# Performance work log

Measured on AMD Instinct MI355X. Metric: run time of the kernel, lower is better.

The kernel has to match this reference:

```python
import jax, jax.numpy as jnp
import numpy as np

B, N, E, Q = 4, 10000, 160000, 256
D, M, U, H, P = 128, 64, 126, 128, 7  # node_dim, msg_sz, update_sz, mlp hidden, pose dim
MSG_STEPS = 3
NUM_COPIES = 1


def setup_inputs() -> dict:
    key = jax.random.key(0)
    ks = jax.random.split(key, 12)
    return {
        "nodes_states": jax.random.normal(ks[0], (B, N, D), jnp.float32),
        "query_poses": jax.random.normal(ks[1], (B, Q, P), jnp.float32),
        "attn": jax.random.uniform(ks[2], (B, Q, N), jnp.float32) / N,
        "edge_sources": jax.random.randint(ks[3], (E,), 0, N),
        "edge_sinks": jax.random.randint(ks[4], (E,), 0, N),
        "w1e": jax.random.normal(ks[5], (2 * D, H), jnp.float32) * 0.05,
        "b1e": jnp.zeros((H,), jnp.float32),
        "w2e": jax.random.normal(ks[6], (H, M), jnp.float32) * 0.05,
        "b2e": jnp.zeros((M,), jnp.float32),
        "w1n": jax.random.normal(ks[7], (D + M, H), jnp.float32) * 0.05,
        "b1n": jnp.zeros((H,), jnp.float32),
        "w2n": jax.random.normal(ks[8], (H, U), jnp.float32) * 0.05,
        "b2n": jnp.zeros((U,), jnp.float32),
    }


def reference(nodes_states, query_poses, attn, edge_sources, edge_sinks,
              w1e, b1e, w2e, b2e, w1n, b1n, w2n, b2n):
    def step(states, _):
        # gather endpoint states: [B, E, 2*D]
        einp = jnp.concatenate([states[:, edge_sources], states[:, edge_sinks]], axis=-1)
        # edge MLP -> per-edge messages [B, E, M]
        msg = jax.nn.relu(einp @ w1e + b1e) @ w2e + b2e
        # scatter-add messages to sink nodes [B, N, M]
        incoming = jnp.zeros((states.shape[0], N, M), states.dtype).at[:, edge_sinks].add(msg)
        # node MLP update [B, N, U]
        ninp = jnp.concatenate([incoming, states], axis=-1)
        upd = jax.nn.relu(ninp @ w1n + b1n) @ w2n + b2n
        # only the last U channels (state part, not positions) are updated
        states = states.at[:, :, -U:].add(upd)
        return states, None

    states, _ = jax.lax.scan(step, nodes_states, None, length=MSG_STEPS)
    extraction = jnp.einsum('bqn,bnd->bqd', attn, states)  # interpolation readout
    return jnp.concatenate([query_poses] * NUM_COPIES + [extraction], axis=-1)
```

## Files before the change

### kernel.cpp

```cpp
#include <hip/hip_runtime.h>

#define Bx 4
#define Nn 10000
#define Ee 160000
#define Qq 256
#define Dd 128
#define Mm 64
#define Uu 126
#define Hh 128
#define Pp 7

#define KG 1252

typedef unsigned short u16;
typedef __bf16 bf16x8 __attribute__((ext_vector_type(8)));
typedef float f32x4 __attribute__((ext_vector_type(4)));

__device__ __forceinline__ float b2f(u16 h){
  unsigned u = ((unsigned)h) << 16; float f; __builtin_memcpy(&f, &u, 4); return f;
}
__device__ __forceinline__ u16 f2b(float f){
  __bf16 h = (__bf16)f; u16 r; __builtin_memcpy(&r, &h, 2); return r;
}
__device__ __forceinline__ float ldin(const void* p, long i, int flag){
  return flag ? b2f(((const u16*)p)[i]) : ((const float*)p)[i];
}

__global__ void probe_kernel(const void* in0, int* flag){
  __shared__ int cnt;
  if (threadIdx.x == 0) cnt = 0;
  __syncthreads();
  float a = fabsf(b2f(((const u16*)in0)[threadIdx.x]));
  if (a > 0.0009765625f && a < 32.0f) atomicAdd(&cnt, 1);
  __syncthreads();
  if (threadIdx.x == 0) *flag = (cnt >= 240) ? 1 : 0;
}

__global__ void prep_init_kernel(const void* w1e, const void* b1e, const void* w2e, const void* b2e,
                                 const void* w1n, const void* b1n, const void* w2n, const void* b2n,
                                 const void* in0, const int* __restrict__ snk,
                                 const int* __restrict__ flag,
                                 u16* w1e_s, u16* w2e_s, u16* w1n_s, u16* w2n_s,
                                 float* b1e_f, float* b2e_f, float* b1n_f, float* b2n_f,
                                 float* __restrict__ sf, u16* __restrict__ sbm,
                                 int* __restrict__ cnt)
{
  int f = *flag;
  long gsz = (long)gridDim.x * blockDim.x;
  long base = (long)blockIdx.x * blockDim.x + threadIdx.x;
  for (long idx = base; idx < 82368; idx += gsz){
    if (idx < 32768){
      int k = (int)idx >> 7, h = (int)idx & 127;
      w1e_s[(k >> 3) * 1024 + h * 8 + (k & 7)] = f2b(ldin(w1e, idx, f));
    } else if (idx < 40960){
      int i2 = (int)idx - 32768; int k = i2 >> 6, m2 = i2 & 63;
      w2e_s[(k >> 3) * 512 + m2 * 8 + (k & 7)] = f2b(ldin(w2e, i2, f));
    } else if (idx < 65536){
      int i2 = (int)idx - 40960; int k = i2 >> 7, h = i2 & 127;
      w1n_s[(k >> 3) * 1024 + h * 8 + (k & 7)] = f2b(ldin(w1n, i2, f));
    } else if (idx < 81920){
      int i2 = (int)idx - 65536; int k = i2 >> 7, u = i2 & 127;
      float v = (u < 126) ? ldin(w2n, (long)k * 126 + u, f) : 0.f;
      w2n_s[(k >> 3) * 1024 + u * 8 + (k & 7)] = f2b(v);
    } else if (idx < 82048){ b1e_f[idx - 81920] = ldin(b1e, idx - 81920, f); }
    else if (idx < 82112){ b2e_f[idx - 82048] = ldin(b2e, idx - 82048, f); }
    else if (idx < 82240){ b1n_f[idx - 82112] = ldin(b1n, idx - 82112, f); }
    else { int j = (int)idx - 82240; b2n_f[j] = (j < 126) ? ldin(b2n, j, f) : 0.f; }
  }
  const long total = (long)Bx * Nn * Dd;
  for (long i = base; i < total; i += gsz){
    float v = ldin(in0, i, f);
    sf[i] = v; sbm[i] = f2b(v);
  }
  for (long i = base; i < Ee; i += gsz)
    atomicAdd(&cnt[snk[(int)i]], 1);
}

__global__ void scan_kernel(const int* __restrict__ cnt, int* __restrict__ rowp){
  __shared__ int tot[1024];
  int t = threadIdx.x;
  int base = t * 10;
  int local[10]; int s = 0;
  #pragma unroll
  for (int i = 0; i < 10; i++){
    int v = (base + i < Nn) ? cnt[base + i] : 0;
    local[i] = s; s += v;
  }
  tot[t] = s;
  __syncthreads();
  for (int o = 1; o < 1024; o <<= 1){
    int v = (t >= o) ? tot[t - o] : 0;
    __syncthreads();
    tot[t] += v;
    __syncthreads();
  }
  int prefix = (t == 0) ? 0 : tot[t - 1];
  #pragma unroll
  for (int i = 0; i < 10; i++)
    if (base + i < Nn) rowp[base + i] = prefix + local[i];
  if (t == 1023) rowp[Nn] = tot[1023];
}
__global__ void fill_kernel(const int* __restrict__ src, const int* __restrict__ snk,
                            const int* __restrict__ rowp, int* __restrict__ cnt,
                            int* __restrict__ psrc){
  int i = blockIdx.x * blockDim.x + threadIdx.x;
  if (i < Ee){
    int s = snk[i];
    int p = rowp[s] + atomicAdd(&cnt[s], 1);
    psrc[p] = src[i];
  }
}

__global__ __launch_bounds__(256) void xform_kernel(
  const u16* __restrict__ sbm, const u16* __restrict__ w1s,
  const float* __restrict__ b1f, u16* __restrict__ xab)
{
  __shared__ __align__(16) u16 w1h[16384];
  __shared__ __align__(16) u16 Yt[64 * 136];
  int tid = threadIdx.x;
  int b = (blockIdx.x & 7) >> 1;
  int nt = ((blockIdx.x >> 3) << 1) + (blockIdx.x & 1);
  if (nt >= 157) return;
  int n0 = nt * 64;
  int w = tid >> 6, lane = tid & 63, m = lane & 15, quad = lane >> 4;
  int n = n0 + w * 16 + m;
  int nld = n < Nn ? n : Nn - 1;
  const u16* srow = sbm + (((size_t)b * Nn + nld) << 7);

  bf16x8 a[4];
  #pragma unroll
  for (int lk = 0; lk < 4; lk++) a[lk] = *(const bf16x8*)(srow + lk * 32 + quad * 8);

  const f32x4 z4 = {0.f, 0.f, 0.f, 0.f};
  int row_l = lane >> 2, seg = lane & 3;
  int nst = n0 + w * 16 + row_l;

  #pragma unroll
  for (int half = 0; half < 2; half++){
    __syncthreads();
    {
      const uint4* g = (const uint4*)(w1s + half * 16384);
      uint4* l = (uint4*)w1h;
      #pragma unroll
      for (int i = 0; i < 8; i++) l[tid + i * 256] = g[tid + i * 256];
    }
    __syncthreads();
    f32x4 acc[8];
    #pragma unroll
    for (int ct = 0; ct < 8; ct++) acc[ct] = z4;
    #pragma unroll
    for (int lk = 0; lk < 4; lk++){
      #pragma unroll
      for (int ct = 0; ct < 8; ct++){
        bf16x8 bv = *(const bf16x8*)(w1h + (((lk * 4 + quad) << 7) + ct * 16 + m) * 8);
        acc[ct] = __builtin_amdgcn_mfma_f32_16x16x32_bf16(a[lk], bv, acc[ct], 0, 0, 0);
      }
    }
    #pragma unroll
    for (int ct = 0; ct < 8; ct++){
      float bb = (half == 0) ? b1f[ct * 16 + m] : 0.f;
      #pragma unroll
      for (int i = 0; i < 4; i++)
        Yt[(w * 16 + quad * 4 + i) * 136 + ct * 16 + m] = f2b(acc[ct][i] + bb);
    }
    if (nst < Nn){
      const u16* tb = Yt + (w * 16 + row_l) * 136 + seg * 8;
      uint4 x0 = *(const uint4*)(tb);
      uint4 x1 = *(const uint4*)(tb + 32);
      uint4 x2 = *(const uint4*)(tb + 64);
      uint4 x3 = *(const uint4*)(tb + 96);
      u16* gb = xab + ((size_t)b * Nn + nst) * 256 + half * 128 + seg * 8;
      *(uint4*)(gb)      = x0;
      *(uint4*)(gb + 32) = x1;
      *(uint4*)(gb + 64) = x2;
      *(uint4*)(gb + 96) = x3;
    }
  }
}

__global__ __launch_bounds__(256) void node_kernel(
  float* __restrict__ sf, u16* __restrict__ sbm, const u16* __restrict__ xab,
  const int* __restrict__ rowp, const int* __restrict__ psrc,
  const u16* __restrict__ w2es, const float* __restrict__ b2ef,
  const u16* __restrict__ w1s, const u16* __restrict__ w2s,
  const float* __restrict__ b1f, const float* __restrict__ b2f2,
  u16* __restrict__ sswz, int last)
{
  __shared__ __align__(16) u16 ninp[64 * 200];
  __shared__ __align__(16) u16 hsYt[64 * 136];
  int b = (blockIdx.x & 7) >> 1;
  int nt = ((blockIdx.x >> 3) << 1) + (blockIdx.x & 1);
  if (nt >= 157) return;
  int n0 = nt * 64;
  int tid = threadIdx.x;

  {
    int nl = tid >> 2, part = tid & 3;
    int n = n0 + nl;
    float acc[32];
    #pragma unroll
    for (int i = 0; i < 32; i++) acc[i] = 0.f;
    if (n < Nn){
      float xbf[32];
      {
        const u16* xp = xab + ((size_t)b * Nn + n) * 256 + 128 + part * 8;
        union { uint4 v; u16 h[8]; } q0, q1, q2, q3;
        q0.v = *(const uint4*)(xp);
        q1.v = *(const uint4*)(xp + 32);
        q2.v = *(const uint4*)(xp + 64);
        q3.v = *(const uint4*)(xp + 96);
        #pragma unroll
        for (int j = 0; j < 8; j++){
          xbf[j] = b2f(q0.h[j]); xbf[8 + j] = b2f(q1.h[j]);
          xbf[16 + j] = b2f(q2.h[j]); xbf[24 + j] = b2f(q3.h[j]);
        }
      }
      int r0 = rowp[n], r1 = rowp[n + 1];
      const u16* xb0 = xab + (size_t)b * Nn * 256 + part * 8;
      for (int r = r0; r < r1; r++){
        int s = psrc[r];
        const u16* xs = xb0 + (size_t)s * 256;
        union { uint4 v; u16 h[8]; } q0, q1, q2, q3;
        q0.v = *(const uint4*)(xs);
        q1.v = *(const uint4*)(xs + 32);
        q2.v = *(const uint4*)(xs + 64);
        q3.v = *(const uint4*)(xs + 96);
        #pragma unroll
        for (int j = 0; j < 8; j++){
          float v0 = b2f(q0.h[j]) + xbf[j];
          acc[j] += v0 > 0.f ? v0 : 0.f;
          float v1 = b2f(q1.h[j]) + xbf[8 + j];
          acc[8 + j] += v1 > 0.f ? v1 : 0.f;
          float v2 = b2f(q2.h[j]) + xbf[16 + j];
          acc[16 + j] += v2 > 0.f ? v2 : 0.f;
          float v3 = b2f(q3.h[j]) + xbf[24 + j];
          acc[24 + j] += v3 > 0.f ? v3 : 0.f;
        }
      }
    }
    union { u16 h[32]; uint4 v[4]; } hb;
    #pragma unroll
    for (int i = 0; i < 32; i++) hb.h[i] = f2b(acc[i]);
    u16* hp = hsYt + nl * 136 + part * 8;
    *(uint4*)(hp)      = hb.v[0];
    *(uint4*)(hp + 32) = hb.v[1];
    *(uint4*)(hp + 64) = hb.v[2];
    *(uint4*)(hp + 96) = hb.v[3];
    u16* dp = ninp + nl * 200 + 64 + part * 8;
    if (n < Nn){
      const u16* sp = sbm + (((size_t)b * Nn + n) << 7) + part * 8;
      *(uint4*)(dp)      = *(const uint4*)(sp);
      *(uint4*)(dp + 32) = *(const uint4*)(sp + 32);
      *(uint4*)(dp + 64) = *(const uint4*)(sp + 64);
      *(uint4*)(dp + 96) = *(const uint4*)(sp + 96);
    } else {
      uint4 zz = {0, 0, 0, 0};
      *(uint4*)(dp)      = zz;
      *(uint4*)(dp + 32) = zz;
      *(uint4*)(dp + 64) = zz;
      *(uint4*)(dp + 96) = zz;
    }
  }

  int w = tid >> 6, lane = tid & 63, m = lane & 15, quad = lane >> 4;
  const f32x4 z4 = {0.f, 0.f, 0.f, 0.f};

  {
    f32x4 acc[4];
    #pragma unroll
    for (int ct = 0; ct < 4; ct++) acc[ct] = z4;
    #pragma unroll
    for (int ks = 0; ks < 4; ks++){
      bf16x8 a = *(const bf16x8*)(hsYt + (w * 16 + m) * 136 + ks * 32 + quad * 8);
      #pragma unroll
      for (int ct = 0; ct < 4; ct++){
        bf16x8 bv = *(const bf16x8*)(w2es + (((ks * 4 + quad) << 6) + ct * 16 + m) * 8);
        acc[ct] = __builtin_amdgcn_mfma_f32_16x16x32_bf16(a, bv, acc[ct], 0, 0, 0);
      }
    }
    #pragma unroll
    for (int i = 0; i < 4; i++){
      int n = n0 + w * 16 + quad * 4 + i;
      float deg = (n < Nn) ? (float)(rowp[n + 1] - rowp[n]) : 0.f;
      #pragma unroll
      for (int ct = 0; ct < 4; ct++)
        ninp[(w * 16 + quad * 4 + i) * 200 + ct * 16 + m] = f2b(acc[ct][i] + deg * b2ef[ct * 16 + m]);
    }
  }

  f32x4 acc1[8];
  #pragma unroll
  for (int ct = 0; ct < 8; ct++) acc1[ct] = z4;
  #pragma unroll 1
  for (int ks = 0; ks < 6; ks++){
    bf16x8 a = *(const bf16x8*)(ninp + (w * 16 + m) * 200 + ks * 32 + quad * 8);
    #pragma unroll
    for (int ct = 0; ct < 8; ct++){
      bf16x8 bv = *(const bf16x8*)(w1s + (((ks * 4 + quad) << 7) + ct * 16 + m) * 8);
      acc1[ct] = __builtin_amdgcn_mfma_f32_16x16x32_bf16(a, bv, acc1[ct], 0, 0, 0);
    }
  }
  #pragma unroll
  for (int ct = 0; ct < 8; ct++){
    float bb = b1f[ct * 16 + m];
    #pragma unroll
    for (int i = 0; i < 4; i++){
      float v = acc1[ct][i] + bb;
      v = v > 0.f ? v : 0.f;
      hsYt[(w * 16 + quad * 4 + i) * 136 + ct * 16 + m] = f2b(v);
    }
  }
  f32x4 acc2[8];
  #pragma unroll
  for (int ct = 0; ct < 8; ct++) acc2[ct] = z4;
  #pragma unroll 1
  for (int ko = 0; ko < 4; ko++){
    bf16x8 a2 = *(const bf16x8*)(hsYt + (w * 16 + m) * 136 + ko * 32 + quad * 8);
    #pragma unroll
    for (int ct = 0; ct < 8; ct++){
      bf16x8 bv = *(const bf16x8*)(w2s + (((ko * 4 + quad) << 7) + ct * 16 + m) * 8);
      acc2[ct] = __builtin_amdgcn_mfma_f32_16x16x32_bf16(a2, bv, acc2[ct], 0, 0, 0);
    }
  }

  #pragma unroll
  for (int ct = 0; ct < 8; ct++){
    int u = ct * 16 + m;
    if (u < 126){
      float bb = b2f2[u];
      #pragma unroll
      for (int i = 0; i < 4; i++){
        int nl = w * 16 + quad * 4 + i;
        int n = n0 + nl;
        if (n < Nn){
          size_t idx = (((size_t)b * Nn + n) << 7) + 2 + u;
          float v = sf[idx] + acc2[ct][i] + bb;
          if (!last){
            sf[idx] = v;
            sbm[idx] = f2b(v);
          } else {
            hsYt[nl * 136 + 2 + u] = f2b(v);
          }
        } else if (last){
          hsYt[nl * 136 + 2 + u] = 0;
        }
      }
    }
  }
  if (last){
    if (m < 2){
      #pragma unroll
      for (int i = 0; i < 4; i++){
        int nl = w * 16 + quad * 4 + i;
        hsYt[nl * 136 + m] = ninp[nl * 200 + 64 + m];
      }
    }
    #pragma unroll
    for (int r = 0; r < 2; r++){
      int kg = nt * 8 + w * 2 + r;
      if (kg < KG){
        #pragma unroll
        for (int dd = 0; dd < 2; dd++){
          int d = dd * 64 + lane;
          union { u16 h[8]; uint4 v; } t;
          #pragma unroll
          for (int j = 0; j < 8; j++) t.h[j] = hsYt[(w * 16 + r * 8 + j) * 136 + d];
          *(uint4*)(sswz + (((size_t)b * KG + kg) * 128 + d) * 8) = t.v;
        }
      }
    }
  }
}

__global__ __launch_bounds__(256) void extract2_kernel(
  const void* __restrict__ attn, const int* __restrict__ flag,
  const u16* __restrict__ sswz, float* __restrict__ part)
{
  int f = *flag;
  int blk = blockIdx.x;
  int kc = blk & 31, qt = (blk >> 5) & 3, b = blk >> 7;
  int tid = threadIdx.x, w = tid >> 6, lane = tid & 63, m = lane & 15, quad = lane >> 4;
  int qr = qt * 4 + w, q0 = qr * 16;
  int kg0 = kc * 40;
  int nsteps = (kc == 31) ? 3 : 10;
  long arow = ((long)(b * Qq + q0 + m)) * Nn;
  const u16* ab16 = (const u16*)attn + arow;
  const float* af32 = (const float*)attn + arow;
  const u16* sbase = sswz + ((size_t)b) * KG * 1024;
  f32x4 acc[8];
  const f32x4 z4 = {0.f, 0.f, 0.f, 0.f};
  #pragma unroll
  for (int ct = 0; ct < 8; ct++) acc[ct] = z4;
  #pragma unroll 2
  for (int t = 0; t < nsteps; t++){
    int kg = kg0 + t * 4 + quad;
    int kgc = kg < KG ? kg : 0;
    bf16x8 a;
    if (kg < 1250){
      if (f){
        a = *(const bf16x8*)(ab16 + kg * 8);
      } else {
        const float* ap = af32 + kg * 8;
        float4 p0 = *(const float4*)ap;
        float4 p1 = *(const float4*)(ap + 4);
        a[0] = (__bf16)p0.x; a[1] = (__bf16)p0.y; a[2] = (__bf16)p0.z; a[3] = (__bf16)p0.w;
        a[4] = (__bf16)p1.x; a[5] = (__bf16)p1.y; a[6] = (__bf16)p1.z; a[7] = (__bf16)p1.w;
      }
    } else {
      #pragma unroll
      for (int j = 0; j < 8; j++) a[j] = (__bf16)0.f;
    }
    #pragma unroll
    for (int ct = 0; ct < 8; ct++){
      bf16x8 bv = *(const bf16x8*)(sbase + ((size_t)kgc * 128 + ct * 16 + m) * 8);
      acc[ct] = __builtin_amdgcn_mfma_f32_16x16x32_bf16(a, bv, acc[ct], 0, 0, 0);
    }
  }
  #pragma unroll
  for (int ct = 0; ct < 8; ct++){
    #pragma unroll
    for (int i = 0; i < 4; i++)
      part[(((size_t)(kc * 4 + b)) * Qq + q0 + quad * 4 + i) * 128 + ct * 16 + m] = acc[ct][i];
  }
}

__global__ void final_kernel(const void* __restrict__ poses, const int* __restrict__ flag,
                             const float* __restrict__ part, void* __restrict__ out)
{
  int f = *flag;
  const long total = (long)Bx * Qq * (Pp + Dd);
  for (long idx = (long)blockIdx.x * blockDim.x + threadIdx.x; idx < total; idx += (long)gridDim.x * blockDim.x){
    int j = (int)(idx % (Pp + Dd));
    long bq = idx / (Pp + Dd);
    float v;
    if (j < Pp){
      v = ldin(poses, bq * Pp + j, f);
    } else {
      int dd = j - Pp;
      int b = (int)(bq >> 8), q = (int)(bq & 255);
      v = 0.f;
      #pragma unroll
      for (int kc = 0; kc < 32; kc++)
        v += part[(((size_t)(kc * 4 + b) * Qq + q) << 7) + dd];
    }
    if (f) ((u16*)out)[idx] = f2b(v);
    else ((float*)out)[idx] = v;
  }
}

extern "C" void kernel_launch(void* const* d_in, const int* in_sizes, int n_in,
                              void* d_out, int out_size, void* d_ws, size_t ws_size,
                              hipStream_t stream)
{
  const void* in_states = d_in[0];
  const void* in_poses  = d_in[1];
  const void* in_attn   = d_in[2];
  const int*  in_src    = (const int*)d_in[3];
  const int*  in_snk    = (const int*)d_in[4];
  const void* in_w1e = d_in[5];  const void* in_b1e = d_in[6];
  const void* in_w2e = d_in[7];  const void* in_b2e = d_in[8];
  const void* in_w1n = d_in[9];  const void* in_b1n = d_in[10];
  const void* in_w2n = d_in[11]; const void* in_b2n = d_in[12];

  char* ws = (char*)d_ws;
  size_t off = 0;
  auto alloc = [&](size_t bytes){ size_t o = off; off = (off + bytes + 255) & ~(size_t)255; return o; };
  size_t o_sf   = alloc((size_t)Bx * Nn * Dd * 4);
  size_t o_sb   = alloc((size_t)Bx * Nn * Dd * 2);
  size_t o_xab  = alloc((size_t)Bx * Nn * 256 * 2);
  size_t o_rowp = alloc((size_t)(Nn + 1) * 4);
  size_t o_rcnt = alloc((size_t)Nn * 2 * 4);
  size_t o_psrc = alloc((size_t)Ee * 4);
  size_t o_w1e  = alloc(32768 * 2);
  size_t o_w2e  = alloc(8192 * 2);
  size_t o_w1n  = alloc(24576 * 2);
  size_t o_w2n  = alloc(16384 * 2);
  size_t o_b1e  = alloc(128 * 4);
  size_t o_b2e  = alloc(64 * 4);
  size_t o_b1n  = alloc(128 * 4);
  size_t o_b2n  = alloc(128 * 4);
  size_t o_flag = alloc(4);

  size_t sswzB = (size_t)Bx * KG * 128 * 8 * 2;
  size_t partB = (size_t)32 * Bx * Qq * Dd * 4;
  size_t o_sswz = alloc(sswzB);
  size_t o_part = alloc(partB);

  float* sf    = (float*)(ws + o_sf);
  u16*   sbm   = (u16*)(ws + o_sb);
  u16*   xab   = (u16*)(ws + o_xab);
  int*   rowp  = (int*)(ws + o_rowp);
  int*   rcnt  = (int*)(ws + o_rcnt);
  int*   rcnt2 = rcnt + Nn;
  int*   psrc  = (int*)(ws + o_psrc);
  u16*   w1e_s = (u16*)(ws + o_w1e);
  u16*   w2e_s = (u16*)(ws + o_w2e);
  u16*   w1n_s = (u16*)(ws + o_w1n);
  u16*   w2n_s = (u16*)(ws + o_w2n);
  float* b1e_f = (float*)(ws + o_b1e);
  float* b2e_f = (float*)(ws + o_b2e);
  float* b1n_f = (float*)(ws + o_b1n);
  float* b2n_f = (float*)(ws + o_b2n);
  int*   flag  = (int*)(ws + o_flag);
  u16*   sswz  = (u16*)(ws + o_sswz);
  float* part  = (float*)(ws + o_part);

  hipMemsetAsync(rcnt, 0, (size_t)Nn * 2 * 4, stream);
  probe_kernel<<<1, 256, 0, stream>>>(in_states, flag);
  prep_init_kernel<<<1024, 256, 0, stream>>>(in_w1e, in_b1e, in_w2e, in_b2e,
                                             in_w1n, in_b1n, in_w2n, in_b2n,
                                             in_states, in_snk, flag,
                                             w1e_s, w2e_s, w1n_s, w2n_s,
                                             b1e_f, b2e_f, b1n_f, b2n_f,
                                             sf, sbm, rcnt);
  scan_kernel<<<1, 1024, 0, stream>>>(rcnt, rowp);
  fill_kernel<<<(Ee + 255) / 256, 256, 0, stream>>>(in_src, in_snk, rowp, rcnt2, psrc);

  for (int step = 0; step < 3; step++){
    xform_kernel<<<632, 256, 0, stream>>>(sbm, w1e_s, b1e_f, xab);
    node_kernel<<<632, 256, 0, stream>>>(sf, sbm, xab, rowp, psrc,
                                         w2e_s, b2e_f,
                                         w1n_s, w2n_s, b1n_f, b2n_f,
                                         sswz, step == 2 ? 1 : 0);
  }
  extract2_kernel<<<512, 256, 0, stream>>>(in_attn, flag, sswz, part);
  final_kernel<<<540, 256, 0, stream>>>(in_poses, flag, part, d_out);
}
```

Baseline: 347.5 us.

## Fuse next-step edge transform into node kernel and atomically reduce readout partials

The per-node first-layer edge projection (xform) for the next message step is now computed at the end of node_kernel from the freshly updated states held in shared memory, using ping-pong xab buffers, so two of the three xform launches and their state reloads go away. xform's shared-memory transpose is replaced by direct packed 16-byte stores, and the readout's 32-way partial buffer becomes atomicAdd into one zeroed sum, which simplifies final_kernel. The w2e swizzle layout also changes. The node kernel gets more shared-memory work and register pressure, and the float atomics make the readout summation order nondeterministic.

New measurement: 340.0 us. 1.02x faster.

```diff
diff --git a/kernel.cpp b/kernel.cpp
--- a/kernel.cpp
+++ b/kernel.cpp
@@ -54,7 +54,7 @@
       w1e_s[(k >> 3) * 1024 + h * 8 + (k & 7)] = f2b(ldin(w1e, idx, f));
     } else if (idx < 40960){
       int i2 = (int)idx - 32768; int k = i2 >> 6, m2 = i2 & 63;
-      w2e_s[(k >> 3) * 512 + m2 * 8 + (k & 7)] = f2b(ldin(w2e, i2, f));
+      w2e_s[(k & 15) * 512 + m2 * 8 + (k >> 4)] = f2b(ldin(w2e, i2, f));
     } else if (idx < 65536){
       int i2 = (int)idx - 40960; int k = i2 >> 7, h = i2 & 127;
       w1n_s[(k >> 3) * 1024 + h * 8 + (k & 7)] = f2b(ldin(w1n, i2, f));
@@ -116,7 +116,6 @@
   const float* __restrict__ b1f, u16* __restrict__ xab)
 {
   __shared__ __align__(16) u16 w1h[16384];
-  __shared__ __align__(16) u16 Yt[64 * 136];
   int tid = threadIdx.x;
   int b = (blockIdx.x & 7) >> 1;
   int nt = ((blockIdx.x >> 3) << 1) + (blockIdx.x & 1);
@@ -132,8 +131,9 @@
   for (int lk = 0; lk < 4; lk++) a[lk] = *(const bf16x8*)(srow + lk * 32 + quad * 8);
 
   const f32x4 z4 = {0.f, 0.f, 0.f, 0.f};
-  int row_l = lane >> 2, seg = lane & 3;
-  int nst = n0 + w * 16 + row_l;
+  float bb[8];
+  #pragma unroll
+  for (int ct = 0; ct < 8; ct++) bb[ct] = b1f[ct * 16 + m];
 
   #pragma unroll
   for (int half = 0; half < 2; half++){
@@ -157,23 +157,15 @@
       }
     }
     #pragma unroll
-    for (int ct = 0; ct < 8; ct++){
-      float bb = (half == 0) ? b1f[ct * 16 + m] : 0.f;
-      #pragma unroll
-      for (int i = 0; i < 4; i++)
-        Yt[(w * 16 + quad * 4 + i) * 136 + ct * 16 + m] = f2b(acc[ct][i] + bb);
-    }
-    if (nst < Nn){
-      const u16* tb = Yt + (w * 16 + row_l) * 136 + seg * 8;
-      uint4 x0 = *(const uint4*)(tb);
-      uint4 x1 = *(const uint4*)(tb + 32);
-      uint4 x2 = *(const uint4*)(tb + 64);
-      uint4 x3 = *(const uint4*)(tb + 96);
-      u16* gb = xab + ((size_t)b * Nn + nst) * 256 + half * 128 + seg * 8;
-      *(uint4*)(gb)      = x0;
-      *(uint4*)(gb + 32) = x1;
-      *(uint4*)(gb + 64) = x2;
-      *(uint4*)(gb + 96) = x3;
+    for (int i = 0; i < 4; i++){
+      int r = n0 + w * 16 + quad * 4 + i;
+      if (r < Nn){
+        union { u16 h[8]; uint4 v; } t;
+        #pragma unroll
+        for (int ct = 0; ct < 8; ct++)
+          t.h[ct] = f2b(acc[ct][i] + ((half == 0) ? bb[ct] : 0.f));
+        *(uint4*)(xab + ((size_t)b * Nn + r) * 256 + half * 128 + m * 8) = t.v;
+      }
     }
   }
 }
@@ -184,7 +176,8 @@
   const u16* __restrict__ w2es, const float* __restrict__ b2ef,
   const u16* __restrict__ w1s, const u16* __restrict__ w2s,
   const float* __restrict__ b1f, const float* __restrict__ b2f2,
-  u16* __restrict__ sswz, int last)
+  const u16* __restrict__ w1es, const float* __restrict__ b1ef,
+  u16* __restrict__ xabn, u16* __restrict__ sswz, int mode)
 {
   __shared__ __align__(16) u16 ninp[64 * 200];
   __shared__ __align__(16) u16 hsYt[64 * 136];
@@ -335,26 +328,64 @@
         if (n < Nn){
           size_t idx = (((size_t)b * Nn + n) << 7) + 2 + u;
           float v = sf[idx] + acc2[ct][i] + bb;
-          if (!last){
+          if (mode == 0){
             sf[idx] = v;
             sbm[idx] = f2b(v);
-          } else {
-            hsYt[nl * 136 + 2 + u] = f2b(v);
           }
-        } else if (last){
+          hsYt[nl * 136 + 2 + u] = f2b(v);
+        } else {
           hsYt[nl * 136 + 2 + u] = 0;
         }
       }
     }
   }
-  if (last){
-    if (m < 2){
+  if (m < 2){
+    #pragma unroll
+    for (int i = 0; i < 4; i++){
+      int nl = w * 16 + quad * 4 + i;
+      hsYt[nl * 136 + m] = ninp[nl * 200 + 64 + m];
+    }
+  }
+
+  if (mode == 0){
+    #pragma unroll
+    for (int half = 0; half < 2; half++){
+      f32x4 xacc[8];
+      #pragma unroll
+      for (int ct = 0; ct < 8; ct++) xacc[ct] = z4;
+      #pragma unroll
+      for (int st = 0; st < 2; st++){
+        __syncthreads();
+        {
+          const uint4* g = (const uint4*)(w1es + half * 16384 + st * 8192);
+          uint4* l = (uint4*)ninp;
+          #pragma unroll
+          for (int i = 0; i < 4; i++) l[tid + i * 256] = g[tid + i * 256];
+        }
+        __syncthreads();
+        #pragma unroll
+        for (int lk = 0; lk < 2; lk++){
+          bf16x8 a = *(const bf16x8*)(hsYt + (w * 16 + m) * 136 + st * 64 + lk * 32 + quad * 8);
+          #pragma unroll
+          for (int ct = 0; ct < 8; ct++){
+            bf16x8 bv = *(const bf16x8*)(ninp + (((lk * 4 + quad) << 7) + ct * 16 + m) * 8);
+            xacc[ct] = __builtin_amdgcn_mfma_f32_16x16x32_bf16(a, bv, xacc[ct], 0, 0, 0);
+          }
+        }
+      }
       #pragma unroll
       for (int i = 0; i < 4; i++){
-        int nl = w * 16 + quad * 4 + i;
-        hsYt[nl * 136 + m] = ninp[nl * 200 + 64 + m];
-      }
-    }
+        int r = n0 + w * 16 + quad * 4 + i;
+        if (r < Nn){
+          union { u16 h[8]; uint4 v; } t;
+          #pragma unroll
+          for (int ct = 0; ct < 8; ct++)
+            t.h[ct] = f2b(xacc[ct][i] + ((half == 0) ? b1ef[ct * 16 + m] : 0.f));
+          *(uint4*)(xabn + ((size_t)b * Nn + r) * 256 + half * 128 + m * 8) = t.v;
+        }
+      }
+    }
+  } else {
     #pragma unroll
     for (int r = 0; r < 2; r++){
       int kg = nt * 8 + w * 2 + r;
@@ -374,7 +405,7 @@
 
 __global__ __launch_bounds__(256) void extract2_kernel(
   const void* __restrict__ attn, const int* __restrict__ flag,
-  const u16* __restrict__ sswz, float* __restrict__ part)
+  const u16* __restrict__ sswz, float* __restrict__ partsum)
 {
   int f = *flag;
   int blk = blockIdx.x;
@@ -420,12 +451,12 @@
   for (int ct = 0; ct < 8; ct++){
     #pragma unroll
     for (int i = 0; i < 4; i++)
-      part[(((size_t)(kc * 4 + b)) * Qq + q0 + quad * 4 + i) * 128 + ct * 16 + m] = acc[ct][i];
+      atomicAdd(&partsum[(((size_t)b * Qq + q0 + quad * 4 + i) << 7) + ct * 16 + m], acc[ct][i]);
   }
 }
 
 __global__ void final_kernel(const void* __restrict__ poses, const int* __restrict__ flag,
-                             const float* __restrict__ part, void* __restrict__ out)
+                             const float* __restrict__ partsum, void* __restrict__ out)
 {
   int f = *flag;
   const long total = (long)Bx * Qq * (Pp + Dd);
@@ -436,12 +467,7 @@
     if (j < Pp){
       v = ldin(poses, bq * Pp + j, f);
     } else {
-      int dd = j - Pp;
-      int b = (int)(bq >> 8), q = (int)(bq & 255);
-      v = 0.f;
-      #pragma unroll
-      for (int kc = 0; kc < 32; kc++)
-        v += part[(((size_t)(kc * 4 + b) * Qq + q) << 7) + dd];
+      v = partsum[(bq << 7) + (j - Pp)];
     }
     if (f) ((u16*)out)[idx] = f2b(v);
     else ((float*)out)[idx] = v;
@@ -465,11 +491,13 @@
   char* ws = (char*)d_ws;
   size_t off = 0;
   auto alloc = [&](size_t bytes){ size_t o = off; off = (off + bytes + 255) & ~(size_t)255; return o; };
+  const size_t psumB = (size_t)Bx * Qq * Dd * 4;
   size_t o_sf   = alloc((size_t)Bx * Nn * Dd * 4);
   size_t o_sb   = alloc((size_t)Bx * Nn * Dd * 2);
-  size_t o_xab  = alloc((size_t)Bx * Nn * 256 * 2);
+  size_t o_xabA = alloc((size_t)Bx * Nn * 256 * 2);
+  size_t o_xabB = alloc((size_t)Bx * Nn * 256 * 2);
   size_t o_rowp = alloc((size_t)(Nn + 1) * 4);
-  size_t o_rcnt = alloc((size_t)Nn * 2 * 4);
+  size_t o_rcnt = alloc((size_t)Nn * 2 * 4 + psumB);
   size_t o_psrc = alloc((size_t)Ee * 4);
   size_t o_w1e  = alloc(32768 * 2);
   size_t o_w2e  = alloc(8192 * 2);
@@ -480,18 +508,16 @@
   size_t o_b1n  = alloc(128 * 4);
   size_t o_b2n  = alloc(128 * 4);
   size_t o_flag = alloc(4);
-
-  size_t sswzB = (size_t)Bx * KG * 128 * 8 * 2;
-  size_t partB = (size_t)32 * Bx * Qq * Dd * 4;
-  size_t o_sswz = alloc(sswzB);
-  size_t o_part = alloc(partB);
+  size_t o_sswz = alloc((size_t)Bx * KG * 128 * 8 * 2);
 
   float* sf    = (float*)(ws + o_sf);
   u16*   sbm   = (u16*)(ws + o_sb);
-  u16*   xab   = (u16*)(ws + o_xab);
+  u16*   xabA  = (u16*)(ws + o_xabA);
+  u16*   xabB  = (u16*)(ws + o_xabB);
   int*   rowp  = (int*)(ws + o_rowp);
   int*   rcnt  = (int*)(ws + o_rcnt);
   int*   rcnt2 = rcnt + Nn;
+  float* psum  = (float*)(ws + o_rcnt + (size_t)Nn * 2 * 4);
   int*   psrc  = (int*)(ws + o_psrc);
   u16*   w1e_s = (u16*)(ws + o_w1e);
   u16*   w2e_s = (u16*)(ws + o_w2e);
@@ -503,9 +529,8 @@
   float* b2n_f = (float*)(ws + o_b2n);
   int*   flag  = (int*)(ws + o_flag);
   u16*   sswz  = (u16*)(ws + o_sswz);
-  float* part  = (float*)(ws + o_part);
-
-  hipMemsetAsync(rcnt, 0, (size_t)Nn * 2 * 4, stream);
+
+  hipMemsetAsync(rcnt, 0, (size_t)Nn * 2 * 4 + psumB, stream);
   probe_kernel<<<1, 256, 0, stream>>>(in_states, flag);
   prep_init_kernel<<<1024, 256, 0, stream>>>(in_w1e, in_b1e, in_w2e, in_b2e,
                                              in_w1n, in_b1n, in_w2n, in_b2n,
@@ -516,13 +541,17 @@
   scan_kernel<<<1, 1024, 0, stream>>>(rcnt, rowp);
   fill_kernel<<<(Ee + 255) / 256, 256, 0, stream>>>(in_src, in_snk, rowp, rcnt2, psrc);
 
-  for (int step = 0; step < 3; step++){
-    xform_kernel<<<632, 256, 0, stream>>>(sbm, w1e_s, b1e_f, xab);
-    node_kernel<<<632, 256, 0, stream>>>(sf, sbm, xab, rowp, psrc,
-                                         w2e_s, b2e_f,
-                                         w1n_s, w2n_s, b1n_f, b2n_f,
-                                         sswz, step == 2 ? 1 : 0);
-  }
-  extract2_kernel<<<512, 256, 0, stream>>>(in_attn, flag, sswz, part);
-  final_kernel<<<540, 256, 0, stream>>>(in_poses, flag, part, d_out);
-}
+  xform_kernel<<<632, 256, 0, stream>>>(sbm, w1e_s, b1e_f, xabA);
+  node_kernel<<<632, 256, 0, stream>>>(sf, sbm, xabA, rowp, psrc,
+                                       w2e_s, b2e_f, w1n_s, w2n_s, b1n_f, b2n_f,
+                                       w1e_s, b1e_f, xabB, sswz, 0);
+  node_kernel<<<632, 256, 0, stream>>>(sf, sbm, xabB, rowp, psrc,
+                                       w2e_s, b2e_f, w1n_s, w2n_s, b1n_f, b2n_f,
+                                       w1e_s, b1e_f, xabA, sswz, 0);
+  node_kernel<<<632, 256, 0, stream>>>(sf, sbm, xabA, rowp, psrc,
+                                       w2e_s, b2e_f, w1n_s, w2n_s, b1n_f, b2n_f,
+                                       w1e_s, b1e_f, xabB, sswz, 1);
+
+  extract2_kernel<<<512, 256, 0, stream>>>(in_attn, flag, sswz, psum);
+  final_kernel<<<540, 256, 0, stream>>>(in_poses, flag, psum, d_out);
+}
```
